# Optimization experiments

Hardware: AMD Instinct MI355X
Metric: run time of the kernel (lower is better)

## Reference

```python
import jax, jax.numpy as jnp
import numpy as np

B, LINES, NREG, D, L, K, CATS = 256, 64, 64, 1024, 64, 16, 2
EPS = 1e-5

_idx = np.arange(K)
# modular digit-wise add / sub mixing tables: M[i,j,m] = 1 iff (i op j) mod K == m
M_ADD = jnp.asarray(((_idx[:, None] + _idx[None, :]) % K)[..., None] == _idx[None, None, :], dtype=jnp.float32)
M_SUB = jnp.asarray(((_idx[:, None] - _idx[None, :]) % K)[..., None] == _idx[None, None, :], dtype=jnp.float32)


def _ln(x, g, b):
    m = x.mean(-1, keepdims=True)
    v = ((x - m) ** 2).mean(-1, keepdims=True)
    return (x - m) / jnp.sqrt(v + EPS) * g + b


def setup_inputs() -> dict:
    key = jax.random.key(0)
    ks = jax.random.split(key, 12)
    p = jax.random.uniform(ks[0], (B, LINES, CATS))
    opcode_probs = p / p.sum(-1, keepdims=True)
    registers = jax.random.normal(ks[1], (B, NREG, D))
    k_write = jax.random.normal(ks[2], (B, LINES, D))
    q_read = jax.random.normal(ks[3], (B, LINES, 2, D))
    cond_distribution = jax.random.uniform(ks[4], (B, LINES, 4))
    gate = jax.random.uniform(ks[5], (B, LINES, 1))
    s = 0.02
    F = L * K
    return {
        'opcode_probs': opcode_probs, 'registers': registers, 'k_write': k_write,
        'q_read': q_read, 'cond_distribution': cond_distribution, 'gate': gate,
        'ln1_g': jnp.ones((D,)), 'ln1_b': jnp.zeros((D,)),
        'w1': jax.random.normal(ks[6], (D, F)) * s, 'b1': jnp.zeros((F,)),
        'ln2_g': jnp.ones((D,)), 'ln2_b': jnp.zeros((D,)),
        'w2': jax.random.normal(ks[7], (D, F)) * s, 'b2': jnp.zeros((F,)),
        'w_res': jax.random.normal(ks[8], (F, D)) * s, 'b_res': jnp.zeros((D,)),
        'lno_g': jnp.ones((D,)), 'lno_b': jnp.zeros((D,)),
    }


def reference(opcode_probs, registers, k_write, q_read, cond_distribution, gate,
              ln1_g, ln1_b, w1, b1, ln2_g, ln2_b, w2, b2, w_res, b_res, lno_g, lno_b):
    scale = 1.0 / jnp.sqrt(jnp.asarray(D, jnp.float32))

    def digit_op(x, y, M):
        # x,y: (b,l,k) digit distributions -> (b,l,k) modular arithmetic result
        return jnp.einsum('bli,blj,ijm->blm', x, y, M)

    def step(R, xs):
        prob, q, kw, g = xs  # (b,2) (b,2,d) (b,d) (b,1)
        # attention read of two operands from register memory
        attn = jax.nn.softmax(jnp.einsum('bqd,brd->bqr', q, R) * scale, axis=-1)
        op_s = jnp.einsum('bqr,brd->bqd', attn, R)
        x = jax.nn.softmax((_ln(op_s[:, 0], ln1_g, ln1_b) @ w1 + b1).reshape(-1, L, K), axis=-1)
        y = jax.nn.softmax((_ln(op_s[:, 1], ln2_g, ln2_b) @ w2 + b2).reshape(-1, L, K), axis=-1)
        outs = jnp.stack([digit_op(x, y, M_ADD), digit_op(x, y, M_SUB)], axis=1)  # (b,2,l,k)
        mix = jnp.einsum('bn,bnlk->blk', prob, outs).reshape(-1, L * K)
        value = _ln(mix @ w_res + b_res, lno_g, lno_b)  # (b,d)
        # attention write-back with gate
        w = jax.nn.softmax(jnp.einsum('bd,brd->br', kw, R) * scale, axis=-1)
        gw = (g * w)[..., None]  # (b,r,1)
        R = R * (1.0 - gw) + gw * value[:, None, :]
        return R, None

    xs = (jnp.moveaxis(opcode_probs, 1, 0), jnp.moveaxis(q_read, 1, 0),
          jnp.moveaxis(k_write, 1, 0), jnp.moveaxis(gate, 1, 0))
    R, _ = jax.lax.scan(step, registers, xs)
    return R
```

## Files before the change

kernel.cpp:

```cpp
#include <hip/hip_runtime.h>
#include <hip/hip_bf16.h>

#define BB 256
#define LINES 64
#define NREG 64
#define DD 1024
#define FF 1024

constexpr float EPS = 1e-5f;
constexpr float SCALE = 0.03125f;

typedef __bf16 bf16_t;
typedef bf16_t bf16x8 __attribute__((ext_vector_type(8)));
typedef unsigned short us16x8 __attribute__((ext_vector_type(8)));
typedef float f32x4 __attribute__((ext_vector_type(4)));
typedef unsigned u32x4v __attribute__((ext_vector_type(4)));
typedef unsigned long long u64;

#define WS_W1T   0u
#define WS_W2T   (2u << 20)
#define WS_WRT   (4u << 20)
#define WS_XNP   (6u << 20)
#define WS_MIXP  (7u << 20)
#define WS_GT    ((7u << 20) + (1u << 19))
#define WS_CTR   ((8u << 20) + (1u << 19))
#define WS_NEED  (WS_CTR + 1024u)

#define SM_WV    0
#define SM_AT0P  256
#define SM_AT1P  512
#define SM_SC0   768
#define SM_SC1   1024
#define SM_SCW   1280
#define SM_RED   1536
#define SM_DYN   2048
#define SM_OSB   SM_DYN
#define SM_AT0   SM_DYN
#define SM_AT1   (SM_DYN + 32768)
#define SM_RED2  (SM_DYN + 65536)
#define SM_PRE   (SM_DYN + 65536 + 13056)
#define SM_VAL   (SM_DYN + 65536 + 13056 + 8448)
#define SM_QPF   (SM_VAL + 4352)
#define SM_SIZE  (SM_QPF + 15360)

__device__ __forceinline__ float wred(float v) {
#pragma unroll
  for (int m = 32; m >= 1; m >>= 1) v += __shfl_xor(v, m);
  return v;
}
__device__ __forceinline__ float wmax64(float v) {
#pragma unroll
  for (int m = 32; m >= 1; m >>= 1) v = fmaxf(v, __shfl_xor(v, m));
  return v;
}

__device__ __forceinline__ void st_llc32(void* p, unsigned v) {
  asm volatile("global_store_dword %0, %1, off sc0 sc1" :: "v"(p), "v"(v) : "memory");
}
__device__ __forceinline__ void st_llc16b(void* p, unsigned short v) {
  unsigned vv = v;
  asm volatile("global_store_short %0, %1, off sc0 sc1" :: "v"(p), "v"(vv) : "memory");
}
__device__ __forceinline__ unsigned ld_llc32(const void* p) {
  unsigned r;
  asm volatile("global_load_dword %0, %1, off sc0 sc1\n\ts_waitcnt vmcnt(0)"
               : "=v"(r) : "v"(p) : "memory");
  return r;
}
__device__ __forceinline__ void ld_llc_4x8_nw(const void* p, u64& a, u64& b, u64& c, u64& d) {
  asm volatile(
      "global_load_dwordx2 %0, %4, off sc0 sc1\n\t"
      "global_load_dwordx2 %1, %4, off offset:8 sc0 sc1\n\t"
      "global_load_dwordx2 %2, %4, off offset:16 sc0 sc1\n\t"
      "global_load_dwordx2 %3, %4, off offset:24 sc0 sc1"
      : "=&v"(a), "=&v"(b), "=&v"(c), "=&v"(d) : "v"(p) : "memory");
}
__device__ __forceinline__ void ld_llc_16_nw(const void* p, u32x4v& r) {
  asm volatile("global_load_dwordx4 %0, %1, off sc0 sc1"
               : "=&v"(r) : "v"(p) : "memory");
}
__device__ __forceinline__ void wait_vm0() {
  asm volatile("s_waitcnt vmcnt(0)" ::: "memory");
  __builtin_amdgcn_sched_barrier(0);
}

__device__ __forceinline__ void group_barrier(unsigned* ctr, int tid, unsigned target) {
  asm volatile("s_waitcnt vmcnt(0)" ::: "memory");
  __syncthreads();
  if (tid == 0) {
    __hip_atomic_fetch_add(ctr, 1u, __ATOMIC_RELAXED, __HIP_MEMORY_SCOPE_AGENT);
    while (ld_llc32(ctr) < target) __builtin_amdgcn_s_sleep(2);
  }
  __syncthreads();
}

__global__ __launch_bounds__(256) void transcvt(const float* __restrict__ w1,
                                                const float* __restrict__ w2,
                                                const float* __restrict__ wr,
                                                bf16_t* __restrict__ out) {
  __shared__ float tl[64][65];
  const float* src = (blockIdx.z == 0) ? w1 : (blockIdx.z == 1) ? w2 : wr;
  bf16_t* dst = out + (size_t)blockIdx.z * (1u << 20);
  const int i0 = blockIdx.x * 64, j0 = blockIdx.y * 64;
  const int t = threadIdx.x;
#pragma unroll
  for (int it = 0; it < 4; ++it) {
    int r = (t >> 4) + it * 16;
    int c4 = (t & 15) * 4;
    const float4 v = *reinterpret_cast<const float4*>(&src[(size_t)(i0 + r) * 1024 + j0 + c4]);
    tl[r][c4] = v.x; tl[r][c4 + 1] = v.y; tl[r][c4 + 2] = v.z; tl[r][c4 + 3] = v.w;
  }
  __syncthreads();
  const int orow = t >> 2, seg = t & 3;
  bf16x8 v0, v1;
#pragma unroll
  for (int u = 0; u < 8; ++u) {
    v0[u] = (bf16_t)tl[seg * 16 + u][orow];
    v1[u] = (bf16_t)tl[seg * 16 + 8 + u][orow];
  }
  bf16_t* dp = dst + (size_t)(j0 + orow) * 1024 + i0 + seg * 16;
  *reinterpret_cast<bf16x8*>(dp) = v0;
  *reinterpret_cast<bf16x8*>(dp + 8) = v1;
}

__global__ __launch_bounds__(1024, 4) void interp3(
    const float* __restrict__ opcode_probs, const float* __restrict__ Rin,
    const float* __restrict__ k_write, const float* __restrict__ q_read,
    const float* __restrict__ gate,
    const float* __restrict__ ln1_g, const float* __restrict__ ln1_b, const float* __restrict__ b1,
    const float* __restrict__ ln2_g, const float* __restrict__ ln2_b, const float* __restrict__ b2,
    const float* __restrict__ b_res, const float* __restrict__ lno_g, const float* __restrict__ lno_b,
    char* __restrict__ ws, float* __restrict__ Rout) {
  __shared__ __align__(16) char smem[SM_SIZE];
  float* wvp  = (float*)(smem + SM_WV);
  float* at0p = (float*)(smem + SM_AT0P);
  float* at1p = (float*)(smem + SM_AT1P);
  float* sc0p = (float*)(smem + SM_SC0);
  float* sc1p = (float*)(smem + SM_SC1);
  float* scwp = (float*)(smem + SM_SCW);
  float* redp = (float*)(smem + SM_RED);

  const int b = blockIdx.x;
  const int g = b >> 4;
  const int j = b & 15;
  const int m = ((b & 7) << 1) | ((b >> 3) & 1);
  const int bq = b;
  const int tid = threadIdx.x;
  const int w = tid >> 6, lane = tid & 63;
  const int ln15 = lane & 15, kgrp = lane >> 4;

  const bf16_t* w1t = (const bf16_t*)(ws + WS_W1T);
  const bf16_t* w2t = (const bf16_t*)(ws + WS_W2T);
  const bf16_t* wrt = (const bf16_t*)(ws + WS_WRT);
  unsigned* xnp   = (unsigned*)(ws + WS_XNP);
  bf16_t*  mixp   = (bf16_t*)(ws + WS_MIXP);
  unsigned* gtw   = (unsigned*)(ws + WS_GT);
  unsigned* ctr   = (unsigned*)(ws + WS_CTR) + g * 16;

  float Rr_[4][16];
  {
    const float* Rsrc = Rin + (size_t)bq * (NREG * DD);
#pragma unroll
    for (int rr = 0; rr < 4; ++rr) {
#pragma unroll
      for (int c = 0; c < 4; ++c) {
        float4 v = *(const float4*)(Rsrc + (size_t)(4 * w + rr) * DD + lane * 16 + c * 4);
        Rr_[rr][c * 4 + 0] = v.x; Rr_[rr][c * 4 + 1] = v.y;
        Rr_[rr][c * 4 + 2] = v.z; Rr_[rr][c * 4 + 3] = v.w;
      }
    }
  }

  {
    const float* qb = q_read + ((size_t)bq * LINES + 0) * (2 * DD);
    const float* kb = k_write + ((size_t)bq * LINES + 0) * DD;
    float* qpf = (float*)(smem + SM_QPF);
    const int pidx = (tid >> 4) * 20 + (tid & 15);
    qpf[pidx] = qb[tid];
    qpf[1280 + pidx] = qb[DD + tid];
    qpf[2560 + pidx] = kb[tid];
  }
  __syncthreads();

  unsigned nbar = 0;

  for (int t = 0; t < LINES; ++t) {
    {
      const float* qpf = (const float*)(smem + SM_QPF);
      const int pb = lane * 20;
#pragma unroll
      for (int v = 0; v < 3; ++v) {
        float* dst = (v == 0) ? sc0p : (v == 1) ? sc1p : scwp;
        float qv[16];
#pragma unroll
        for (int c = 0; c < 4; ++c) {
          float4 t4 = *(const float4*)(qpf + v * 1280 + pb + c * 4);
          qv[c * 4 + 0] = t4.x; qv[c * 4 + 1] = t4.y;
          qv[c * 4 + 2] = t4.z; qv[c * 4 + 3] = t4.w;
        }
#pragma unroll
        for (int rr = 0; rr < 4; ++rr) {
          float s = 0.f;
#pragma unroll
          for (int jj = 0; jj < 16; ++jj) s = fmaf(Rr_[rr][jj], qv[jj], s);
          s = wred(s);
          if (lane == 0) dst[4 * w + rr] = s * SCALE;
        }
      }
    }
    __syncthreads();
    if (w < 3) {
      const float* src = (w == 0) ? sc0p : (w == 1) ? sc1p : scwp;
      float* dst = (w == 0) ? at0p : (w == 1) ? at1p : wvp;
      float v = src[lane];
      float mx = wmax64(v);
      float e = expf(v - mx);
      float s = wred(e);
      dst[lane] = e / s;
    }
    __syncthreads();
    float os0, os1;
    {
      float p0[16], p1[16];
#pragma unroll
      for (int jj = 0; jj < 16; ++jj) { p0[jj] = 0.f; p1[jj] = 0.f; }
#pragma unroll
      for (int rr = 0; rr < 4; ++rr) {
        float a0 = at0p[4 * w + rr], a1 = at1p[4 * w + rr];
#pragma unroll
        for (int jj = 0; jj < 16; ++jj) {
          p0[jj] = fmaf(a0, Rr_[rr][jj], p0[jj]);
          p1[jj] = fmaf(a1, Rr_[rr][jj], p1[jj]);
        }
      }
      float* osb = (float*)(smem + SM_OSB);
      const int rp = (tid >> 4) * 17 + (tid & 15);
#pragma unroll
      for (int jj = 0; jj < 16; ++jj) osb[w * 1088 + lane * 17 + jj] = p0[jj];
      __syncthreads();
      os0 = 0.f;
#pragma unroll
      for (int ww = 0; ww < 16; ++ww) os0 += osb[ww * 1088 + rp];
      __syncthreads();
#pragma unroll
      for (int jj = 0; jj < 16; ++jj) osb[w * 1088 + lane * 17 + jj] = p1[jj];
      __syncthreads();
      os1 = 0.f;
#pragma unroll
      for (int ww = 0; ww < 16; ++ww) os1 += osb[ww * 1088 + rp];
    }
    {
      float s0 = wred(os0), qq0 = wred(os0 * os0);
      float s1 = wred(os1), qq1 = wred(os1 * os1);
      if (lane == 0) { redp[w*4] = s0; redp[w*4+1] = qq0; redp[w*4+2] = s1; redp[w*4+3] = qq1; }
      __syncthreads();
      float S0 = 0, Q0 = 0, S1 = 0, Q1 = 0;
#pragma unroll
      for (int i = 0; i < 16; ++i) { S0 += redp[i*4]; Q0 += redp[i*4+1]; S1 += redp[i*4+2]; Q1 += redp[i*4+3]; }
      float m0 = S0 * (1.f / DD), v0 = fmaxf(Q0 * (1.f / DD) - m0 * m0, 0.f);
      float m1 = S1 * (1.f / DD), v1 = fmaxf(Q1 * (1.f / DD) - m1 * m1, 0.f);
      float xn0v = (os0 - m0) * rsqrtf(v0 + EPS) * ln1_g[tid] + ln1_b[tid];
      float xn1v = (os1 - m1) * rsqrtf(v1 + EPS) * ln2_g[tid] + ln2_b[tid];
      unsigned pw = (unsigned)__builtin_bit_cast(unsigned short, (bf16_t)xn0v)
                  | ((unsigned)__builtin_bit_cast(unsigned short, (bf16_t)xn1v) << 16);
      st_llc32(&xnp[((size_t)g * 16 + j) * DD + tid], pw);
    }
    group_barrier(ctr, tid, 16u * (++nbar));

    {
      const char* base = (const char*)(xnp + (size_t)g * (16 * DD));
      const int row = tid >> 7, k16 = tid & 127;
      u64 a0, a1, a2, a3, c0, c1, c2, c3;
      ld_llc_4x8_nw(base + (size_t)row * 4096 + k16 * 32, a0, a1, a2, a3);
      ld_llc_4x8_nw(base + (size_t)(row + 8) * 4096 + k16 * 32, c0, c1, c2, c3);
      wait_vm0();
#pragma unroll
      for (int h = 0; h < 2; ++h) {
        u64 x0 = h ? c0 : a0, x1 = h ? c1 : a1, x2 = h ? c2 : a2, x3 = h ? c3 : a3;
        int r = row + h * 8;
        us16x8 v0, v1;
        v0[0] = (unsigned short)x0;         v1[0] = (unsigned short)(x0 >> 16);
        v0[1] = (unsigned short)(x0 >> 32); v1[1] = (unsigned short)(x0 >> 48);
        v0[2] = (unsigned short)x1;         v1[2] = (unsigned short)(x1 >> 16);
        v0[3] = (unsigned short)(x1 >> 32); v1[3] = (unsigned short)(x1 >> 48);
        v0[4] = (unsigned short)x2;         v1[4] = (unsigned short)(x2 >> 16);
        v0[5] = (unsigned short)(x2 >> 32); v1[5] = (unsigned short)(x2 >> 48);
        v0[6] = (unsigned short)x3;         v1[6] = (unsigned short)(x3 >> 16);
        v0[7] = (unsigned short)(x3 >> 32); v1[7] = (unsigned short)(x3 >> 48);
        unsigned byte = (unsigned)(r * 2048 + k16 * 16) ^ ((unsigned)(r & 7) << 4);
        *(us16x8*)(smem + SM_AT0 + byte) = v0;
        *(us16x8*)(smem + SM_AT1 + byte) = v1;
      }
    }
    float pf0, pf1, pf2;
    {
      int tn = (t + 1 < LINES) ? (t + 1) : (LINES - 1);
      const float* qb2 = q_read + ((size_t)bq * LINES + tn) * (2 * DD);
      const float* kb2 = k_write + ((size_t)bq * LINES + tn) * DD;
      pf0 = qb2[tid]; pf1 = qb2[DD + tid]; pf2 = kb2[tid];
    }
    __syncthreads();

#pragma unroll
    for (int gm = 0; gm < 2; ++gm) {
      const char* atile = smem + (gm ? SM_AT1 : SM_AT0);
      const int ns = w & 3, ks = w >> 2;
      const bf16_t* bsrc = (gm ? w2t : w1t) + (size_t)(64 * m + ns * 16 + ln15) * DD;
      f32x4 acc = {0.f, 0.f, 0.f, 0.f};
#pragma unroll
      for (int kc = 0; kc < 8; ++kc) {
        int kb = ks * 256 + kc * 32 + kgrp * 8;
        unsigned abyte = ((unsigned)(ln15 * 2048 + kb * 2)) ^ ((unsigned)(ln15 & 7) << 4);
        bf16x8 av = *(const bf16x8*)(atile + abyte);
        bf16x8 bv = *(const bf16x8*)(bsrc + kb);
        acc = __builtin_amdgcn_mfma_f32_16x16x32_bf16(av, bv, acc, 0, 0, 0);
      }
      __syncthreads();
      float* red2 = (float*)(smem + SM_RED2);
      if (ks > 0) {
#pragma unroll
        for (int r2 = 0; r2 < 4; ++r2)
          red2[((ks - 1) * 4 + ns) * (16 * 17) + (kgrp * 4 + r2) * 17 + ln15] = acc[r2];
      }
      __syncthreads();
      if (ks == 0) {
        float* prep = (float*)(smem + SM_PRE) + gm * (16 * 66);
#pragma unroll
        for (int r2 = 0; r2 < 4; ++r2) {
          int crow = kgrp * 4 + r2;
          float v = acc[r2];
#pragma unroll
          for (int kk = 0; kk < 3; ++kk)
            v += red2[(kk * 4 + ns) * (16 * 17) + crow * 17 + ln15];
          prep[crow * 66 + ns * 16 + ln15] = v;
        }
      }
      __syncthreads();
    }
    {
      float* prep = (float*)(smem + SM_PRE);
      const int bb2 = w, c = lane;
      float xp = prep[bb2 * 66 + c] + b1[64 * m + c];
      float yp = prep[16 * 66 + bb2 * 66 + c] + b2[64 * m + c];
      float mx1 = xp, mx2 = yp;
#pragma unroll
      for (int msk = 1; msk < 16; msk <<= 1) {
        mx1 = fmaxf(mx1, __shfl_xor(mx1, msk));
        mx2 = fmaxf(mx2, __shfl_xor(mx2, msk));
      }
      float e1 = expf(xp - mx1), e2 = expf(yp - mx2);
      float s1 = e1, s2 = e2;
#pragma unroll
      for (int msk = 1; msk < 16; msk <<= 1) {
        s1 += __shfl_xor(s1, msk);
        s2 += __shfl_xor(s2, msk);
      }
      float x = e1 / s1, y = e2 / s2;
      int mm = lane & 15, basel = lane & ~15;
      float addv = 0.f, subv = 0.f;
#pragma unroll
      for (int i = 0; i < 16; ++i) {
        float xi = __shfl(x, basel + i);
        float ya = __shfl(y, basel + ((mm - i) & 15));
        float ys = __shfl(y, basel + ((i - mm) & 15));
        addv = fmaf(xi, ya, addv);
        subv = fmaf(xi, ys, subv);
      }
      int q2 = g * 16 + bb2;
      const float* pr = opcode_probs + ((size_t)q2 * LINES + t) * 2;
      float mix = pr[0] * addv + pr[1] * subv;
      st_llc16b(&mixp[((size_t)g * 16 + bb2) * DD + 64 * m + c],
                __builtin_bit_cast(unsigned short, (bf16_t)mix));
    }
    group_barrier(ctr, tid, 16u * (++nbar));

    {
      const char* base = (const char*)(mixp + (size_t)g * (16 * DD));
      const int row = tid >> 7, k16 = tid & 127;
      u32x4v va, vb;
      ld_llc_16_nw(base + (size_t)row * 2048 + k16 * 16, va);
      ld_llc_16_nw(base + (size_t)(row + 8) * 2048 + k16 * 16, vb);
      wait_vm0();
      unsigned byte0 = (unsigned)(row * 2048 + k16 * 16) ^ ((unsigned)(row & 7) << 4);
      unsigned byte1 = (unsigned)((row + 8) * 2048 + k16 * 16) ^ ((unsigned)(row & 7) << 4);
      *(u32x4v*)(smem + SM_AT0 + byte0) = va;
      *(u32x4v*)(smem + SM_AT0 + byte1) = vb;
      __syncthreads();
      const int ns = w & 3, ks = w >> 2;
      const bf16_t* bsrc = wrt + (size_t)(64 * m + ns * 16 + ln15) * DD;
      f32x4 acc = {0.f, 0.f, 0.f, 0.f};
#pragma unroll
      for (int kc = 0; kc < 8; ++kc) {
        int kb = ks * 256 + kc * 32 + kgrp * 8;
        unsigned abyte = ((unsigned)(ln15 * 2048 + kb * 2)) ^ ((unsigned)(ln15 & 7) << 4);
        bf16x8 av = *(const bf16x8*)(smem + SM_AT0 + abyte);
        bf16x8 bv = *(const bf16x8*)(bsrc + kb);
        acc = __builtin_amdgcn_mfma_f32_16x16x32_bf16(av, bv, acc, 0, 0, 0);
      }
      __syncthreads();
      float* red2 = (float*)(smem + SM_RED2);
      if (ks > 0) {
#pragma unroll
        for (int r2 = 0; r2 < 4; ++r2)
          red2[((ks - 1) * 4 + ns) * (16 * 17) + (kgrp * 4 + r2) * 17 + ln15] = acc[r2];
      }
      __syncthreads();
      if (ks == 0) {
        int f = 64 * m + ns * 16 + ln15;
#pragma unroll
        for (int r2 = 0; r2 < 4; ++r2) {
          int crow = kgrp * 4 + r2;
          float v = acc[r2];
#pragma unroll
          for (int kk = 0; kk < 3; ++kk)
            v += red2[(kk * 4 + ns) * (16 * 17) + crow * 17 + ln15];
          st_llc32(&gtw[((size_t)g * 16 + crow) * DD + f],
                   __builtin_bit_cast(unsigned, v + b_res[f]));
        }
      }
    }
    group_barrier(ctr, tid, 16u * (++nbar));

    {
      float xv = __builtin_bit_cast(float, ld_llc32(&gtw[((size_t)g * 16 + j) * DD + tid]));
      float s1 = wred(xv), s2 = wred(xv * xv);
      if (lane == 0) { redp[w * 2] = s1; redp[w * 2 + 1] = s2; }
      __syncthreads();
      float S = 0.f, Q = 0.f;
#pragma unroll
      for (int i = 0; i < 16; ++i) { S += redp[i * 2]; Q += redp[i * 2 + 1]; }
      float mn = S * (1.f / DD), vr = fmaxf(Q * (1.f / DD) - mn * mn, 0.f);
      float vv = (xv - mn) * rsqrtf(vr + EPS) * lno_g[tid] + lno_b[tid];
      float* valp = (float*)(smem + SM_VAL);
      valp[(tid >> 4) * 17 + (tid & 15)] = vv;
    }
    __syncthreads();
    {
      float gtv = gate[(size_t)bq * LINES + t];
      const float* valp = (const float*)(smem + SM_VAL);
      float vvj[16];
#pragma unroll
      for (int jj = 0; jj < 16; ++jj) vvj[jj] = valp[lane * 17 + jj];
#pragma unroll
      for (int rr = 0; rr < 4; ++rr) {
        float gg = gtv * wvp[4 * w + rr];
#pragma unroll
        for (int jj = 0; jj < 16; ++jj)
          Rr_[rr][jj] = Rr_[rr][jj] * (1.f - gg) + gg * vvj[jj];
      }
      float* qpf = (float*)(smem + SM_QPF);
      const int pidx = (tid >> 4) * 20 + (tid & 15);
      qpf[pidx] = pf0;
      qpf[1280 + pidx] = pf1;
      qpf[2560 + pidx] = pf2;
    }
    __syncthreads();
  }

  {
    float* Rdst = Rout + (size_t)bq * (NREG * DD);
#pragma unroll
    for (int rr = 0; rr < 4; ++rr) {
#pragma unroll
      for (int c = 0; c < 4; ++c) {
        float4 v;
        v.x = Rr_[rr][c * 4 + 0]; v.y = Rr_[rr][c * 4 + 1];
        v.z = Rr_[rr][c * 4 + 2]; v.w = Rr_[rr][c * 4 + 3];
        *(float4*)(Rdst + (size_t)(4 * w + rr) * DD + lane * 16 + c * 4) = v;
      }
    }
  }
}

__global__ __launch_bounds__(1024) void interp_fb(
    const float* __restrict__ opcode_probs, const float* __restrict__ k_write,
    const float* __restrict__ q_read, const float* __restrict__ gate,
    const float* __restrict__ ln1_g, const float* __restrict__ ln1_b,
    const float* __restrict__ w1, const float* __restrict__ b1,
    const float* __restrict__ ln2_g, const float* __restrict__ ln2_b,
    const float* __restrict__ w2, const float* __restrict__ b2,
    const float* __restrict__ w_res, const float* __restrict__ b_res,
    const float* __restrict__ lno_g, const float* __restrict__ lno_b,
    float* __restrict__ R) {
  __shared__ float q0s[DD], q1s[DD], kws[DD];
  __shared__ float sc0[NREG], sc1[NREG], scw[NREG];
  __shared__ float at0[NREG], at1[NREG], wv[NREG];
  __shared__ float xn0[DD], xn1[DD];
  __shared__ float mixs[FF];
  __shared__ float val[DD];
  __shared__ float red[64];
  const int b = blockIdx.x;
  const int tid = threadIdx.x;
  const int w = tid >> 6, lane = tid & 63;
  float* Rb = R + (size_t)b * NREG * DD;
  for (int t = 0; t < LINES; ++t) {
    const float* qb = q_read + ((size_t)b * LINES + t) * 2 * DD;
    const float* kb = k_write + ((size_t)b * LINES + t) * DD;
    q0s[tid] = qb[tid]; q1s[tid] = qb[DD + tid]; kws[tid] = kb[tid];
    __syncthreads();
#pragma unroll
    for (int rr = 0; rr < 4; ++rr) {
      int r = w * 4 + rr;
      const float* Rr = Rb + (size_t)r * DD;
      float a0 = 0.f, a1 = 0.f, aw = 0.f;
#pragma unroll
      for (int jj = 0; jj < 16; ++jj) {
        int d = jj * 64 + lane;
        float rv = Rr[d];
        a0 += rv * q0s[d]; a1 += rv * q1s[d]; aw += rv * kws[d];
      }
      a0 = wred(a0); a1 = wred(a1); aw = wred(aw);
      if (lane == 0) { sc0[r] = a0 * SCALE; sc1[r] = a1 * SCALE; scw[r] = aw * SCALE; }
    }
    __syncthreads();
    if (w < 3) {
      const float* src = (w == 0) ? sc0 : (w == 1) ? sc1 : scw;
      float* dst = (w == 0) ? at0 : (w == 1) ? at1 : wv;
      float v = src[lane];
      float mx = wmax64(v);
      float e = expf(v - mx);
      float s = wred(e);
      dst[lane] = e / s;
    }
    __syncthreads();
    float os0 = 0.f, os1 = 0.f;
#pragma unroll 4
    for (int r = 0; r < NREG; ++r) {
      float rv = Rb[(size_t)r * DD + tid];
      os0 += at0[r] * rv; os1 += at1[r] * rv;
    }
    {
      float s0 = wred(os0), qq0 = wred(os0 * os0);
      float s1 = wred(os1), qq1 = wred(os1 * os1);
      if (lane == 0) { red[w*4] = s0; red[w*4+1] = qq0; red[w*4+2] = s1; red[w*4+3] = qq1; }
      __syncthreads();
      float S0 = 0, Q0 = 0, S1 = 0, Q1 = 0;
#pragma unroll
      for (int i = 0; i < 16; ++i) { S0 += red[i*4]; Q0 += red[i*4+1]; S1 += red[i*4+2]; Q1 += red[i*4+3]; }
      float m0 = S0 / DD, v0 = fmaxf(Q0 / DD - m0 * m0, 0.f);
      float m1 = S1 / DD, v1 = fmaxf(Q1 / DD - m1 * m1, 0.f);
      xn0[tid] = (os0 - m0) * rsqrtf(v0 + EPS) * ln1_g[tid] + ln1_b[tid];
      xn1[tid] = (os1 - m1) * rsqrtf(v1 + EPS) * ln2_g[tid] + ln2_b[tid];
      __syncthreads();
    }
    float p1v = b1[tid], p2v = b2[tid];
    {
      const float* c1 = w1 + tid;
      const float* c2 = w2 + tid;
#pragma unroll 4
      for (int d = 0; d < DD; ++d) {
        p1v += xn0[d] * c1[(size_t)d * FF];
        p2v += xn1[d] * c2[(size_t)d * FF];
      }
    }
    {
      int mmm = lane & 15, basel = lane & ~15;
      float mx1 = p1v, mx2 = p2v;
      for (int msk = 1; msk < 16; msk <<= 1) {
        mx1 = fmaxf(mx1, __shfl_xor(mx1, msk));
        mx2 = fmaxf(mx2, __shfl_xor(mx2, msk));
      }
      float e1 = expf(p1v - mx1), e2 = expf(p2v - mx2);
      float s1 = e1, s2 = e2;
      for (int msk = 1; msk < 16; msk <<= 1) { s1 += __shfl_xor(s1, msk); s2 += __shfl_xor(s2, msk); }
      float x = e1 / s1, y = e2 / s2;
      float addv = 0.f, subv = 0.f;
#pragma unroll
      for (int i = 0; i < 16; ++i) {
        float xi = __shfl(x, basel + i);
        float ya = __shfl(y, basel + ((mmm - i) & 15));
        float ys = __shfl(y, basel + ((i - mmm) & 15));
        addv += xi * ya; subv += xi * ys;
      }
      const float* pr = opcode_probs + ((size_t)b * LINES + t) * 2;
      mixs[tid] = pr[0] * addv + pr[1] * subv;
    }
    __syncthreads();
    float acc = b_res[tid];
    {
      const float* cr = w_res + tid;
#pragma unroll 4
      for (int f = 0; f < FF; ++f) acc += mixs[f] * cr[(size_t)f * DD];
    }
    {
      float s1 = wred(acc), s2 = wred(acc * acc);
      if (lane == 0) { red[w*2] = s1; red[w*2+1] = s2; }
      __syncthreads();
      float S = 0, Q = 0;
#pragma unroll
      for (int i = 0; i < 16; ++i) { S += red[i*2]; Q += red[i*2+1]; }
      float mn = S / DD, vr = fmaxf(Q / DD - mn * mn, 0.f);
      val[tid] = (acc - mn) * rsqrtf(vr + EPS) * lno_g[tid] + lno_b[tid];
      __syncthreads();
    }
    {
      float gt_ = gate[(size_t)b * LINES + t];
      float vv = val[tid];
#pragma unroll 4
      for (int r = 0; r < NREG; ++r) {
        float gg = gt_ * wv[r];
        size_t idx = (size_t)r * DD + tid;
        Rb[idx] = Rb[idx] * (1.f - gg) + gg * vv;
      }
    }
    __syncthreads();
  }
}

extern "C" void kernel_launch(void* const* d_in, const int* in_sizes, int n_in,
                              void* d_out, int out_size, void* d_ws, size_t ws_size,
                              hipStream_t stream) {
  const float* opcode = (const float*)d_in[0];
  const float* registers = (const float*)d_in[1];
  const float* k_write = (const float*)d_in[2];
  const float* q_read = (const float*)d_in[3];
  const float* gate = (const float*)d_in[5];
  const float* ln1_g = (const float*)d_in[6];
  const float* ln1_b = (const float*)d_in[7];
  const float* w1 = (const float*)d_in[8];
  const float* b1 = (const float*)d_in[9];
  const float* ln2_g = (const float*)d_in[10];
  const float* ln2_b = (const float*)d_in[11];
  const float* w2 = (const float*)d_in[12];
  const float* b2 = (const float*)d_in[13];
  const float* w_res = (const float*)d_in[14];
  const float* b_res = (const float*)d_in[15];
  const float* lno_g = (const float*)d_in[16];
  const float* lno_b = (const float*)d_in[17];
  float* R = (float*)d_out;

  if (ws_size >= (size_t)WS_NEED) {
    transcvt<<<dim3(16, 16, 3), 256, 0, stream>>>(w1, w2, w_res, (bf16_t*)d_ws);
    hipMemsetAsync((char*)d_ws + WS_CTR, 0, 1024, stream);
    interp3<<<BB, 1024, 0, stream>>>(opcode, registers, k_write, q_read, gate,
                                     ln1_g, ln1_b, b1, ln2_g, ln2_b, b2,
                                     b_res, lno_g, lno_b, (char*)d_ws, R);
  } else {
    hipMemcpyAsync(R, registers, (size_t)BB * NREG * DD * sizeof(float),
                   hipMemcpyDeviceToDevice, stream);
    interp_fb<<<BB, 1024, 0, stream>>>(opcode, k_write, q_read, gate, ln1_g, ln1_b,
                                       w1, b1, ln2_g, ln2_b, w2, b2, w_res, b_res,
                                       lno_g, lno_b, R);
  }
}
```

Baseline: 3.953 ms.

## Replace atomic group counter with per-block flags and remap block-to-group assignment

The group barrier no longer has thread 0 atomically increment a shared counter and spin on it. Each block now writes its own flag slot with a monotonically increasing tag, and one wavefront polls all 16 flags and exits once every flag has reached the tag. Group membership changes from contiguous block IDs to interleaved ones (g = b&15, j = b>>4), so the 16 blocks of a group are spread across the device. The next-step prefetch of q/k is issued earlier, and two syncthreads before the split-K reduction are removed, relying on the LDS regions used there not overlapping.

```diff
diff --git a/kernel.cpp b/kernel.cpp
--- a/kernel.cpp
+++ b/kernel.cpp
@@ -84,12 +84,16 @@
   __builtin_amdgcn_sched_barrier(0);
 }
 
-__device__ __forceinline__ void group_barrier(unsigned* ctr, int tid, unsigned target) {
+__device__ __forceinline__ void group_barrier(unsigned* flg, int tid, int m, unsigned tag) {
   asm volatile("s_waitcnt vmcnt(0)" ::: "memory");
   __syncthreads();
-  if (tid == 0) {
-    __hip_atomic_fetch_add(ctr, 1u, __ATOMIC_RELAXED, __HIP_MEMORY_SCOPE_AGENT);
-    while (ld_llc32(ctr) < target) __builtin_amdgcn_s_sleep(2);
+  if (tid < 64) {
+    if (tid == 0) st_llc32(&flg[m], tag);
+    for (;;) {
+      unsigned v = (tid < 16) ? ld_llc32(&flg[tid]) : tag;
+      if (__all(v >= tag)) break;
+      __builtin_amdgcn_s_sleep(2);
+    }
   }
   __syncthreads();
 }
@@ -141,9 +145,9 @@
   float* redp = (float*)(smem + SM_RED);
 
   const int b = blockIdx.x;
-  const int g = b >> 4;
-  const int j = b & 15;
-  const int m = ((b & 7) << 1) | ((b >> 3) & 1);
+  const int g = b & 15;
+  const int j = b >> 4;
+  const int m = j;
   const int bq = b;
   const int tid = threadIdx.x;
   const int w = tid >> 6, lane = tid & 63;
@@ -155,7 +159,7 @@
   unsigned* xnp   = (unsigned*)(ws + WS_XNP);
   bf16_t*  mixp   = (bf16_t*)(ws + WS_MIXP);
   unsigned* gtw   = (unsigned*)(ws + WS_GT);
-  unsigned* ctr   = (unsigned*)(ws + WS_CTR) + g * 16;
+  unsigned* flg   = (unsigned*)(ws + WS_CTR) + g * 16;
 
   float Rr_[4][16];
   {
@@ -218,6 +222,13 @@
       float s = wred(e);
       dst[lane] = e / s;
     }
+    float pf0, pf1, pf2;
+    {
+      int tn = (t + 1 < LINES) ? (t + 1) : (LINES - 1);
+      const float* qb2 = q_read + ((size_t)bq * LINES + tn) * (2 * DD);
+      const float* kb2 = k_write + ((size_t)bq * LINES + tn) * DD;
+      pf0 = qb2[tid]; pf1 = qb2[DD + tid]; pf2 = kb2[tid];
+    }
     __syncthreads();
     float os0, os1;
     {
@@ -265,7 +276,7 @@
                   | ((unsigned)__builtin_bit_cast(unsigned short, (bf16_t)xn1v) << 16);
       st_llc32(&xnp[((size_t)g * 16 + j) * DD + tid], pw);
     }
-    group_barrier(ctr, tid, 16u * (++nbar));
+    group_barrier(flg, tid, m, ++nbar);
 
     {
       const char* base = (const char*)(xnp + (size_t)g * (16 * DD));
@@ -292,13 +303,6 @@
         *(us16x8*)(smem + SM_AT1 + byte) = v1;
       }
     }
-    float pf0, pf1, pf2;
-    {
-      int tn = (t + 1 < LINES) ? (t + 1) : (LINES - 1);
-      const float* qb2 = q_read + ((size_t)bq * LINES + tn) * (2 * DD);
-      const float* kb2 = k_write + ((size_t)bq * LINES + tn) * DD;
-      pf0 = qb2[tid]; pf1 = qb2[DD + tid]; pf2 = kb2[tid];
-    }
     __syncthreads();
 
 #pragma unroll
@@ -315,7 +319,6 @@
         bf16x8 bv = *(const bf16x8*)(bsrc + kb);
         acc = __builtin_amdgcn_mfma_f32_16x16x32_bf16(av, bv, acc, 0, 0, 0);
       }
-      __syncthreads();
       float* red2 = (float*)(smem + SM_RED2);
       if (ks > 0) {
 #pragma unroll
@@ -366,13 +369,13 @@
         addv = fmaf(xi, ya, addv);
         subv = fmaf(xi, ys, subv);
       }
-      int q2 = g * 16 + bb2;
+      int q2 = (bb2 << 4) | g;
       const float* pr = opcode_probs + ((size_t)q2 * LINES + t) * 2;
       float mix = pr[0] * addv + pr[1] * subv;
       st_llc16b(&mixp[((size_t)g * 16 + bb2) * DD + 64 * m + c],
                 __builtin_bit_cast(unsigned short, (bf16_t)mix));
     }
-    group_barrier(ctr, tid, 16u * (++nbar));
+    group_barrier(flg, tid, m, ++nbar);
 
     {
       const char* base = (const char*)(mixp + (size_t)g * (16 * DD));
@@ -397,7 +400,6 @@
         bf16x8 bv = *(const bf16x8*)(bsrc + kb);
         acc = __builtin_amdgcn_mfma_f32_16x16x32_bf16(av, bv, acc, 0, 0, 0);
       }
-      __syncthreads();
       float* red2 = (float*)(smem + SM_RED2);
       if (ks > 0) {
 #pragma unroll
@@ -419,7 +421,7 @@
         }
       }
     }
-    group_barrier(ctr, tid, 16u * (++nbar));
+    group_barrier(flg, tid, m, ++nbar);
 
     {
       float xv = __builtin_bit_cast(float, ld_llc32(&gtw[((size_t)g * 16 + j) * DD + tid]));
```

Result: slower. 4.062 ms (+2.8%).

## Replace cross-block grouped MFMA GEMMs with per-block scalar GEMV

Applied to the files above, without the earlier changes.

Drops the design where 16 blocks cooperate on MFMA GEMMs through global workspace and spin-wait group barriers. Each block now computes its own batch row's three 1024x1024 matvecs with bf16 weights streamed from global/L2 and fp32 FMAs, reducing partial sums in shared memory. This removes the inter-block atomic barriers and the global round-trips each step. In exchange, every block re-reads the full weight matrices each step (16x more weight traffic), drops tensor-core use, and no longer prefetches the next step's q/k inputs.

```diff
diff --git a/kernel.cpp b/kernel.cpp
--- a/kernel.cpp
+++ b/kernel.cpp
@@ -11,37 +11,27 @@
 constexpr float SCALE = 0.03125f;
 
 typedef __bf16 bf16_t;
-typedef bf16_t bf16x8 __attribute__((ext_vector_type(8)));
-typedef unsigned short us16x8 __attribute__((ext_vector_type(8)));
-typedef float f32x4 __attribute__((ext_vector_type(4)));
 typedef unsigned u32x4v __attribute__((ext_vector_type(4)));
-typedef unsigned long long u64;
-
-#define WS_W1T   0u
-#define WS_W2T   (2u << 20)
-#define WS_WRT   (4u << 20)
-#define WS_XNP   (6u << 20)
-#define WS_MIXP  (7u << 20)
-#define WS_GT    ((7u << 20) + (1u << 19))
-#define WS_CTR   ((8u << 20) + (1u << 19))
-#define WS_NEED  (WS_CTR + 1024u)
-
-#define SM_WV    0
-#define SM_AT0P  256
-#define SM_AT1P  512
-#define SM_SC0   768
-#define SM_SC1   1024
-#define SM_SCW   1280
-#define SM_RED   1536
-#define SM_DYN   2048
-#define SM_OSB   SM_DYN
-#define SM_AT0   SM_DYN
-#define SM_AT1   (SM_DYN + 32768)
-#define SM_RED2  (SM_DYN + 65536)
-#define SM_PRE   (SM_DYN + 65536 + 13056)
-#define SM_VAL   (SM_DYN + 65536 + 13056 + 8448)
-#define SM_QPF   (SM_VAL + 4352)
-#define SM_SIZE  (SM_QPF + 15360)
+
+#define WS_W1   0u
+#define WS_W2   (2u << 20)
+#define WS_WR   (4u << 20)
+#define WS_NEED (6u << 20)
+
+#define SM_WV     0
+#define SM_AT0P   256
+#define SM_AT1P   512
+#define SM_SC0    768
+#define SM_SC1    1024
+#define SM_SCW    1280
+#define SM_RED    1536
+#define SM_XN0    2048
+#define SM_XN1    6144
+#define SM_SCRATCH 10240
+#define SM_MIX    79872
+#define SM_VAL    83968
+#define SM_QPF    88320
+#define SM_SIZE   103680
 
 __device__ __forceinline__ float wred(float v) {
 #pragma unroll
@@ -53,84 +43,33 @@
   for (int m = 32; m >= 1; m >>= 1) v = fmaxf(v, __shfl_xor(v, m));
   return v;
 }
-
-__device__ __forceinline__ void st_llc32(void* p, unsigned v) {
-  asm volatile("global_store_dword %0, %1, off sc0 sc1" :: "v"(p), "v"(v) : "memory");
-}
-__device__ __forceinline__ void st_llc16b(void* p, unsigned short v) {
-  unsigned vv = v;
-  asm volatile("global_store_short %0, %1, off sc0 sc1" :: "v"(p), "v"(vv) : "memory");
-}
-__device__ __forceinline__ unsigned ld_llc32(const void* p) {
-  unsigned r;
-  asm volatile("global_load_dword %0, %1, off sc0 sc1\n\ts_waitcnt vmcnt(0)"
-               : "=v"(r) : "v"(p) : "memory");
-  return r;
-}
-__device__ __forceinline__ void ld_llc_4x8_nw(const void* p, u64& a, u64& b, u64& c, u64& d) {
-  asm volatile(
-      "global_load_dwordx2 %0, %4, off sc0 sc1\n\t"
-      "global_load_dwordx2 %1, %4, off offset:8 sc0 sc1\n\t"
-      "global_load_dwordx2 %2, %4, off offset:16 sc0 sc1\n\t"
-      "global_load_dwordx2 %3, %4, off offset:24 sc0 sc1"
-      : "=&v"(a), "=&v"(b), "=&v"(c), "=&v"(d) : "v"(p) : "memory");
-}
-__device__ __forceinline__ void ld_llc_16_nw(const void* p, u32x4v& r) {
-  asm volatile("global_load_dwordx4 %0, %1, off sc0 sc1"
-               : "=&v"(r) : "v"(p) : "memory");
-}
-__device__ __forceinline__ void wait_vm0() {
-  asm volatile("s_waitcnt vmcnt(0)" ::: "memory");
-  __builtin_amdgcn_sched_barrier(0);
-}
-
-__device__ __forceinline__ void group_barrier(unsigned* ctr, int tid, unsigned target) {
-  asm volatile("s_waitcnt vmcnt(0)" ::: "memory");
-  __syncthreads();
-  if (tid == 0) {
-    __hip_atomic_fetch_add(ctr, 1u, __ATOMIC_RELAXED, __HIP_MEMORY_SCOPE_AGENT);
-    while (ld_llc32(ctr) < target) __builtin_amdgcn_s_sleep(2);
-  }
-  __syncthreads();
-}
-
-__global__ __launch_bounds__(256) void transcvt(const float* __restrict__ w1,
-                                                const float* __restrict__ w2,
-                                                const float* __restrict__ wr,
-                                                bf16_t* __restrict__ out) {
-  __shared__ float tl[64][65];
-  const float* src = (blockIdx.z == 0) ? w1 : (blockIdx.z == 1) ? w2 : wr;
-  bf16_t* dst = out + (size_t)blockIdx.z * (1u << 20);
-  const int i0 = blockIdx.x * 64, j0 = blockIdx.y * 64;
-  const int t = threadIdx.x;
-#pragma unroll
-  for (int it = 0; it < 4; ++it) {
-    int r = (t >> 4) + it * 16;
-    int c4 = (t & 15) * 4;
-    const float4 v = *reinterpret_cast<const float4*>(&src[(size_t)(i0 + r) * 1024 + j0 + c4]);
-    tl[r][c4] = v.x; tl[r][c4 + 1] = v.y; tl[r][c4 + 2] = v.z; tl[r][c4 + 3] = v.w;
-  }
-  __syncthreads();
-  const int orow = t >> 2, seg = t & 3;
-  bf16x8 v0, v1;
-#pragma unroll
-  for (int u = 0; u < 8; ++u) {
-    v0[u] = (bf16_t)tl[seg * 16 + u][orow];
-    v1[u] = (bf16_t)tl[seg * 16 + 8 + u][orow];
-  }
-  bf16_t* dp = dst + (size_t)(j0 + orow) * 1024 + i0 + seg * 16;
-  *reinterpret_cast<bf16x8*>(dp) = v0;
-  *reinterpret_cast<bf16x8*>(dp + 8) = v1;
-}
-
-__global__ __launch_bounds__(1024, 4) void interp3(
+__device__ __forceinline__ float bflo(unsigned u) {
+  return __builtin_bit_cast(float, u << 16);
+}
+__device__ __forceinline__ float bfhi(unsigned u) {
+  return __builtin_bit_cast(float, u & 0xffff0000u);
+}
+
+__global__ __launch_bounds__(1024) void cvt3(const float* __restrict__ w1,
+                                             const float* __restrict__ w2,
+                                             const float* __restrict__ wr,
+                                             bf16_t* __restrict__ o) {
+  const int bz = blockIdx.x >> 8;
+  const int off = ((blockIdx.x & 255) * 1024 + threadIdx.x) * 4;
+  const float* src = (bz == 0) ? w1 : (bz == 1) ? w2 : wr;
+  float4 v = *(const float4*)(src + off);
+  bf16_t* dp = o + ((size_t)bz << 20) + off;
+  dp[0] = (bf16_t)v.x; dp[1] = (bf16_t)v.y; dp[2] = (bf16_t)v.z; dp[3] = (bf16_t)v.w;
+}
+
+__global__ __launch_bounds__(1024, 4) void interp4(
     const float* __restrict__ opcode_probs, const float* __restrict__ Rin,
     const float* __restrict__ k_write, const float* __restrict__ q_read,
     const float* __restrict__ gate,
     const float* __restrict__ ln1_g, const float* __restrict__ ln1_b, const float* __restrict__ b1,
     const float* __restrict__ ln2_g, const float* __restrict__ ln2_b, const float* __restrict__ b2,
     const float* __restrict__ b_res, const float* __restrict__ lno_g, const float* __restrict__ lno_b,
-    char* __restrict__ ws, float* __restrict__ Rout) {
+    const char* __restrict__ ws, float* __restrict__ Rout) {
   __shared__ __align__(16) char smem[SM_SIZE];
   float* wvp  = (float*)(smem + SM_WV);
   float* at0p = (float*)(smem + SM_AT0P);
@@ -139,23 +78,17 @@
   float* sc1p = (float*)(smem + SM_SC1);
   float* scwp = (float*)(smem + SM_SCW);
   float* redp = (float*)(smem + SM_RED);
-
-  const int b = blockIdx.x;
-  const int g = b >> 4;
-  const int j = b & 15;
-  const int m = ((b & 7) << 1) | ((b >> 3) & 1);
-  const int bq = b;
+  float* xn0L = (float*)(smem + SM_XN0);
+  float* xn1L = (float*)(smem + SM_XN1);
+  float* mixL = (float*)(smem + SM_MIX);
+
+  const int bq = blockIdx.x;
   const int tid = threadIdx.x;
   const int w = tid >> 6, lane = tid & 63;
-  const int ln15 = lane & 15, kgrp = lane >> 4;
-
-  const bf16_t* w1t = (const bf16_t*)(ws + WS_W1T);
-  const bf16_t* w2t = (const bf16_t*)(ws + WS_W2T);
-  const bf16_t* wrt = (const bf16_t*)(ws + WS_WRT);
-  unsigned* xnp   = (unsigned*)(ws + WS_XNP);
-  bf16_t*  mixp   = (bf16_t*)(ws + WS_MIXP);
-  unsigned* gtw   = (unsigned*)(ws + WS_GT);
-  unsigned* ctr   = (unsigned*)(ws + WS_CTR) + g * 16;
+
+  const bf16_t* w1b = (const bf16_t*)(ws + WS_W1);
+  const bf16_t* w2b = (const bf16_t*)(ws + WS_W2);
+  const bf16_t* wrb = (const bf16_t*)(ws + WS_WR);
 
   float Rr_[4][16];
   {
@@ -171,20 +104,17 @@
     }
   }
 
-  {
-    const float* qb = q_read + ((size_t)bq * LINES + 0) * (2 * DD);
-    const float* kb = k_write + ((size_t)bq * LINES + 0) * DD;
-    float* qpf = (float*)(smem + SM_QPF);
-    const int pidx = (tid >> 4) * 20 + (tid & 15);
-    qpf[pidx] = qb[tid];
-    qpf[1280 + pidx] = qb[DD + tid];
-    qpf[2560 + pidx] = kb[tid];
-  }
-  __syncthreads();
-
-  unsigned nbar = 0;
-
   for (int t = 0; t < LINES; ++t) {
+    {
+      const float* qb = q_read + ((size_t)bq * LINES + t) * (2 * DD);
+      const float* kb = k_write + ((size_t)bq * LINES + t) * DD;
+      float* qpf = (float*)(smem + SM_QPF);
+      const int pidx = (tid >> 4) * 20 + (tid & 15);
+      qpf[pidx] = qb[tid];
+      qpf[1280 + pidx] = qb[DD + tid];
+      qpf[2560 + pidx] = kb[tid];
+    }
+    __syncthreads();
     {
       const float* qpf = (const float*)(smem + SM_QPF);
       const int pb = lane * 20;
@@ -233,7 +163,7 @@
           p1[jj] = fmaf(a1, Rr_[rr][jj], p1[jj]);
         }
       }
-      float* osb = (float*)(smem + SM_OSB);
+      float* osb = (float*)(smem + SM_SCRATCH);
       const int rp = (tid >> 4) * 17 + (tid & 15);
 #pragma unroll
       for (int jj = 0; jj < 16; ++jj) osb[w * 1088 + lane * 17 + jj] = p0[jj];
@@ -259,96 +189,58 @@
       for (int i = 0; i < 16; ++i) { S0 += redp[i*4]; Q0 += redp[i*4+1]; S1 += redp[i*4+2]; Q1 += redp[i*4+3]; }
       float m0 = S0 * (1.f / DD), v0 = fmaxf(Q0 * (1.f / DD) - m0 * m0, 0.f);
       float m1 = S1 * (1.f / DD), v1 = fmaxf(Q1 * (1.f / DD) - m1 * m1, 0.f);
-      float xn0v = (os0 - m0) * rsqrtf(v0 + EPS) * ln1_g[tid] + ln1_b[tid];
-      float xn1v = (os1 - m1) * rsqrtf(v1 + EPS) * ln2_g[tid] + ln2_b[tid];
-      unsigned pw = (unsigned)__builtin_bit_cast(unsigned short, (bf16_t)xn0v)
-                  | ((unsigned)__builtin_bit_cast(unsigned short, (bf16_t)xn1v) << 16);
-      st_llc32(&xnp[((size_t)g * 16 + j) * DD + tid], pw);
-    }
-    group_barrier(ctr, tid, 16u * (++nbar));
-
-    {
-      const char* base = (const char*)(xnp + (size_t)g * (16 * DD));
-      const int row = tid >> 7, k16 = tid & 127;
-      u64 a0, a1, a2, a3, c0, c1, c2, c3;
-      ld_llc_4x8_nw(base + (size_t)row * 4096 + k16 * 32, a0, a1, a2, a3);
-      ld_llc_4x8_nw(base + (size_t)(row + 8) * 4096 + k16 * 32, c0, c1, c2, c3);
-      wait_vm0();
-#pragma unroll
-      for (int h = 0; h < 2; ++h) {
-        u64 x0 = h ? c0 : a0, x1 = h ? c1 : a1, x2 = h ? c2 : a2, x3 = h ? c3 : a3;
-        int r = row + h * 8;
-        us16x8 v0, v1;
-        v0[0] = (unsigned short)x0;         v1[0] = (unsigned short)(x0 >> 16);
-        v0[1] = (unsigned short)(x0 >> 32); v1[1] = (unsigned short)(x0 >> 48);
-        v0[2] = (unsigned short)x1;         v1[2] = (unsigned short)(x1 >> 16);
-        v0[3] = (unsigned short)(x1 >> 32); v1[3] = (unsigned short)(x1 >> 48);
-        v0[4] = (unsigned short)x2;         v1[4] = (unsigned short)(x2 >> 16);
-        v0[5] = (unsigned short)(x2 >> 32); v1[5] = (unsigned short)(x2 >> 48);
-        v0[6] = (unsigned short)x3;         v1[6] = (unsigned short)(x3 >> 16);
-        v0[7] = (unsigned short)(x3 >> 32); v1[7] = (unsigned short)(x3 >> 48);
-        unsigned byte = (unsigned)(r * 2048 + k16 * 16) ^ ((unsigned)(r & 7) << 4);
-        *(us16x8*)(smem + SM_AT0 + byte) = v0;
-        *(us16x8*)(smem + SM_AT1 + byte) = v1;
-      }
-    }
-    float pf0, pf1, pf2;
-    {
-      int tn = (t + 1 < LINES) ? (t + 1) : (LINES - 1);
-      const float* qb2 = q_read + ((size_t)bq * LINES + tn) * (2 * DD);
-      const float* kb2 = k_write + ((size_t)bq * LINES + tn) * DD;
-      pf0 = qb2[tid]; pf1 = qb2[DD + tid]; pf2 = kb2[tid];
-    }
-    __syncthreads();
-
-#pragma unroll
-    for (int gm = 0; gm < 2; ++gm) {
-      const char* atile = smem + (gm ? SM_AT1 : SM_AT0);
-      const int ns = w & 3, ks = w >> 2;
-      const bf16_t* bsrc = (gm ? w2t : w1t) + (size_t)(64 * m + ns * 16 + ln15) * DD;
-      f32x4 acc = {0.f, 0.f, 0.f, 0.f};
-#pragma unroll
-      for (int kc = 0; kc < 8; ++kc) {
-        int kb = ks * 256 + kc * 32 + kgrp * 8;
-        unsigned abyte = ((unsigned)(ln15 * 2048 + kb * 2)) ^ ((unsigned)(ln15 & 7) << 4);
-        bf16x8 av = *(const bf16x8*)(atile + abyte);
-        bf16x8 bv = *(const bf16x8*)(bsrc + kb);
-        acc = __builtin_amdgcn_mfma_f32_16x16x32_bf16(av, bv, acc, 0, 0, 0);
-      }
-      __syncthreads();
-      float* red2 = (float*)(smem + SM_RED2);
-      if (ks > 0) {
-#pragma unroll
-        for (int r2 = 0; r2 < 4; ++r2)
-          red2[((ks - 1) * 4 + ns) * (16 * 17) + (kgrp * 4 + r2) * 17 + ln15] = acc[r2];
-      }
-      __syncthreads();
-      if (ks == 0) {
-        float* prep = (float*)(smem + SM_PRE) + gm * (16 * 66);
-#pragma unroll
-        for (int r2 = 0; r2 < 4; ++r2) {
-          int crow = kgrp * 4 + r2;
-          float v = acc[r2];
-#pragma unroll
-          for (int kk = 0; kk < 3; ++kk)
-            v += red2[(kk * 4 + ns) * (16 * 17) + crow * 17 + ln15];
-          prep[crow * 66 + ns * 16 + ln15] = v;
+      xn0L[tid] = (os0 - m0) * rsqrtf(v0 + EPS) * ln1_g[tid] + ln1_b[tid];
+      xn1L[tid] = (os1 - m1) * rsqrtf(v1 + EPS) * ln2_g[tid] + ln2_b[tid];
+    }
+    __syncthreads();
+
+    float p1v, p2v;
+    {
+      const int dg = w >> 1, fh = w & 1;
+      const float* x0p = xn0L + dg * 128;
+      const float* x1p = xn1L + dg * 128;
+      const bf16_t* wp1 = w1b + ((size_t)dg * 128 * FF) + fh * 512 + lane * 8;
+      const bf16_t* wp2 = w2b + ((size_t)dg * 128 * FF) + fh * 512 + lane * 8;
+      float acc0[8], acc1[8];
+#pragma unroll
+      for (int k = 0; k < 8; ++k) { acc0[k] = 0.f; acc1[k] = 0.f; }
+#pragma unroll 4
+      for (int i = 0; i < 128; ++i) {
+        float x0 = x0p[i], x1 = x1p[i];
+        u32x4v u1 = *(const u32x4v*)(wp1 + (size_t)i * FF);
+        u32x4v u2 = *(const u32x4v*)(wp2 + (size_t)i * FF);
+#pragma unroll
+        for (int c = 0; c < 4; ++c) {
+          acc0[2*c]   = fmaf(bflo(u1[c]), x0, acc0[2*c]);
+          acc0[2*c+1] = fmaf(bfhi(u1[c]), x0, acc0[2*c+1]);
+          acc1[2*c]   = fmaf(bflo(u2[c]), x1, acc1[2*c]);
+          acc1[2*c+1] = fmaf(bfhi(u2[c]), x1, acc1[2*c+1]);
         }
       }
-      __syncthreads();
-    }
-    {
-      float* prep = (float*)(smem + SM_PRE);
-      const int bb2 = w, c = lane;
-      float xp = prep[bb2 * 66 + c] + b1[64 * m + c];
-      float yp = prep[16 * 66 + bb2 * 66 + c] + b2[64 * m + c];
-      float mx1 = xp, mx2 = yp;
+      float* part = (float*)(smem + SM_SCRATCH);
+      float* dst = part + dg * 1024 + fh * 512 + lane * 8;
+#pragma unroll
+      for (int k = 0; k < 8; ++k) dst[k] = acc0[k];
+      __syncthreads();
+      p1v = b1[tid];
+#pragma unroll
+      for (int k = 0; k < 8; ++k) p1v += part[k * 1024 + tid];
+      __syncthreads();
+#pragma unroll
+      for (int k = 0; k < 8; ++k) dst[k] = acc1[k];
+      __syncthreads();
+      p2v = b2[tid];
+#pragma unroll
+      for (int k = 0; k < 8; ++k) p2v += part[k * 1024 + tid];
+    }
+    {
+      float mx1 = p1v, mx2 = p2v;
 #pragma unroll
       for (int msk = 1; msk < 16; msk <<= 1) {
         mx1 = fmaxf(mx1, __shfl_xor(mx1, msk));
         mx2 = fmaxf(mx2, __shfl_xor(mx2, msk));
       }
-      float e1 = expf(xp - mx1), e2 = expf(yp - mx2);
+      float e1 = expf(p1v - mx1), e2 = expf(p2v - mx2);
       float s1 = e1, s2 = e2;
 #pragma unroll
       for (int msk = 1; msk < 16; msk <<= 1) {
@@ -366,71 +258,46 @@
         addv = fmaf(xi, ya, addv);
         subv = fmaf(xi, ys, subv);
       }
-      int q2 = g * 16 + bb2;
-      const float* pr = opcode_probs + ((size_t)q2 * LINES + t) * 2;
-      float mix = pr[0] * addv + pr[1] * subv;
-      st_llc16b(&mixp[((size_t)g * 16 + bb2) * DD + 64 * m + c],
-                __builtin_bit_cast(unsigned short, (bf16_t)mix));
-    }
-    group_barrier(ctr, tid, 16u * (++nbar));
-
-    {
-      const char* base = (const char*)(mixp + (size_t)g * (16 * DD));
-      const int row = tid >> 7, k16 = tid & 127;
-      u32x4v va, vb;
-      ld_llc_16_nw(base + (size_t)row * 2048 + k16 * 16, va);
-      ld_llc_16_nw(base + (size_t)(row + 8) * 2048 + k16 * 16, vb);
-      wait_vm0();
-      unsigned byte0 = (unsigned)(row * 2048 + k16 * 16) ^ ((unsigned)(row & 7) << 4);
-      unsigned byte1 = (unsigned)((row + 8) * 2048 + k16 * 16) ^ ((unsigned)(row & 7) << 4);
-      *(u32x4v*)(smem + SM_AT0 + byte0) = va;
-      *(u32x4v*)(smem + SM_AT0 + byte1) = vb;
-      __syncthreads();
-      const int ns = w & 3, ks = w >> 2;
-      const bf16_t* bsrc = wrt + (size_t)(64 * m + ns * 16 + ln15) * DD;
-      f32x4 acc = {0.f, 0.f, 0.f, 0.f};
-#pragma unroll
-      for (int kc = 0; kc < 8; ++kc) {
-        int kb = ks * 256 + kc * 32 + kgrp * 8;
-        unsigned abyte = ((unsigned)(ln15 * 2048 + kb * 2)) ^ ((unsigned)(ln15 & 7) << 4);
-        bf16x8 av = *(const bf16x8*)(smem + SM_AT0 + abyte);
-        bf16x8 bv = *(const bf16x8*)(bsrc + kb);
-        acc = __builtin_amdgcn_mfma_f32_16x16x32_bf16(av, bv, acc, 0, 0, 0);
-      }
-      __syncthreads();
-      float* red2 = (float*)(smem + SM_RED2);
-      if (ks > 0) {
-#pragma unroll
-        for (int r2 = 0; r2 < 4; ++r2)
-          red2[((ks - 1) * 4 + ns) * (16 * 17) + (kgrp * 4 + r2) * 17 + ln15] = acc[r2];
-      }
-      __syncthreads();
-      if (ks == 0) {
-        int f = 64 * m + ns * 16 + ln15;
-#pragma unroll
-        for (int r2 = 0; r2 < 4; ++r2) {
-          int crow = kgrp * 4 + r2;
-          float v = acc[r2];
-#pragma unroll
-          for (int kk = 0; kk < 3; ++kk)
-            v += red2[(kk * 4 + ns) * (16 * 17) + crow * 17 + ln15];
-          st_llc32(&gtw[((size_t)g * 16 + crow) * DD + f],
-                   __builtin_bit_cast(unsigned, v + b_res[f]));
+      const float* pr = opcode_probs + ((size_t)bq * LINES + t) * 2;
+      mixL[tid] = pr[0] * addv + pr[1] * subv;
+    }
+    __syncthreads();
+    float gacc;
+    {
+      const int kg = w >> 1, dh = w & 1;
+      const float* xp = mixL + kg * 128;
+      const bf16_t* wp = wrb + ((size_t)kg * 128 * DD) + dh * 512 + lane * 8;
+      float acc[8];
+#pragma unroll
+      for (int k = 0; k < 8; ++k) acc[k] = 0.f;
+#pragma unroll 4
+      for (int i = 0; i < 128; ++i) {
+        float x = xp[i];
+        u32x4v u = *(const u32x4v*)(wp + (size_t)i * DD);
+#pragma unroll
+        for (int c = 0; c < 4; ++c) {
+          acc[2*c]   = fmaf(bflo(u[c]), x, acc[2*c]);
+          acc[2*c+1] = fmaf(bfhi(u[c]), x, acc[2*c+1]);
         }
       }
-    }
-    group_barrier(ctr, tid, 16u * (++nbar));
-
-    {
-      float xv = __builtin_bit_cast(float, ld_llc32(&gtw[((size_t)g * 16 + j) * DD + tid]));
-      float s1 = wred(xv), s2 = wred(xv * xv);
+      float* part = (float*)(smem + SM_SCRATCH);
+      float* dst = part + kg * 1024 + dh * 512 + lane * 8;
+#pragma unroll
+      for (int k = 0; k < 8; ++k) dst[k] = acc[k];
+      __syncthreads();
+      gacc = b_res[tid];
+#pragma unroll
+      for (int k = 0; k < 8; ++k) gacc += part[k * 1024 + tid];
+    }
+    {
+      float s1 = wred(gacc), s2 = wred(gacc * gacc);
       if (lane == 0) { redp[w * 2] = s1; redp[w * 2 + 1] = s2; }
       __syncthreads();
       float S = 0.f, Q = 0.f;
 #pragma unroll
       for (int i = 0; i < 16; ++i) { S += redp[i * 2]; Q += redp[i * 2 + 1]; }
       float mn = S * (1.f / DD), vr = fmaxf(Q * (1.f / DD) - mn * mn, 0.f);
-      float vv = (xv - mn) * rsqrtf(vr + EPS) * lno_g[tid] + lno_b[tid];
+      float vv = (gacc - mn) * rsqrtf(vr + EPS) * lno_g[tid] + lno_b[tid];
       float* valp = (float*)(smem + SM_VAL);
       valp[(tid >> 4) * 17 + (tid & 15)] = vv;
     }
@@ -448,11 +315,6 @@
         for (int jj = 0; jj < 16; ++jj)
           Rr_[rr][jj] = Rr_[rr][jj] * (1.f - gg) + gg * vvj[jj];
       }
-      float* qpf = (float*)(smem + SM_QPF);
-      const int pidx = (tid >> 4) * 20 + (tid & 15);
-      qpf[pidx] = pf0;
-      qpf[1280 + pidx] = pf1;
-      qpf[2560 + pidx] = pf2;
     }
     __syncthreads();
   }
@@ -630,11 +492,10 @@
   float* R = (float*)d_out;
 
   if (ws_size >= (size_t)WS_NEED) {
-    transcvt<<<dim3(16, 16, 3), 256, 0, stream>>>(w1, w2, w_res, (bf16_t*)d_ws);
-    hipMemsetAsync((char*)d_ws + WS_CTR, 0, 1024, stream);
-    interp3<<<BB, 1024, 0, stream>>>(opcode, registers, k_write, q_read, gate,
+    cvt3<<<768, 1024, 0, stream>>>(w1, w2, w_res, (bf16_t*)d_ws);
+    interp4<<<BB, 1024, 0, stream>>>(opcode, registers, k_write, q_read, gate,
                                      ln1_g, ln1_b, b1, ln2_g, ln2_b, b2,
-                                     b_res, lno_g, lno_b, (char*)d_ws, R);
+                                     b_res, lno_g, lno_b, (const char*)d_ws, R);
   } else {
     hipMemcpyAsync(R, registers, (size_t)BB * NREG * DD * sizeof(float),
                    hipMemcpyDeviceToDevice, stream);
```

Result: slower. 6.505 ms (+64.5%).
